# Kernel tuning notes

Measured on AMD Instinct MI355X. Metric: run time of the kernel, lower is better.

## Reference

```python
import jax, jax.numpy as jnp
import numpy as np


def setup_inputs() -> dict:
    key = jax.random.key(0)
    k1, k2 = jax.random.split(key)
    B, H, W, C = 8, 384, 1280, 8
    U = jax.random.normal(k1, (B, H, W, C), dtype=jnp.float32)
    flo = jax.random.normal(k2, (B, H, W, 2), dtype=jnp.float32)
    return {"U": U, "flo": flo}


def _forward_warp(U, flo):
    # Faithful port of transformerFwd: bilinear forward splatting.
    B, H, W, C = U.shape
    out_h, out_w = H, W  # out_size == (H, W) as used in get_occlusion_mask_from_flow
    # normalized sampling grid in [-1, 1]
    x_s = jnp.linspace(-1.0, 1.0, out_w, dtype=jnp.float32)  # [W]
    y_s = jnp.linspace(-1.0, 1.0, out_h, dtype=jnp.float32)  # [H]
    x_t = x_s[None, None, :] + flo[..., 0] / ((out_w - 1.0) / 2.0)  # [B,H,W]
    y_t = y_s[None, :, None] + flo[..., 1] / ((out_h - 1.0) / 2.0)  # [B,H,W]
    # map back to pixel coords
    x = (x_t.reshape(-1) + 1.0) * (W - 1.0) / 2.0  # [B*H*W]
    y = (y_t.reshape(-1) + 1.0) * (H - 1.0) / 2.0
    x0 = jnp.floor(x).astype(jnp.int32)
    x1 = x0 + 1
    y0 = jnp.floor(y).astype(jnp.int32)
    y1 = y0 + 1
    x0c = jnp.clip(x0, 0, W - 1)
    x1c = jnp.clip(x1, 0, W - 1)
    y0c = jnp.clip(y0, 0, H - 1)
    y1c = jnp.clip(y1, 0, H - 1)
    # flat destination indices into [B*H*W]
    base = jnp.repeat(jnp.arange(B, dtype=jnp.int32) * (H * W), out_h * out_w)
    idx_a = base + y0c * W + x0c
    idx_b = base + y1c * W + x0c
    idx_c = base + y0c * W + x1c
    idx_d = base + y1c * W + x1c
    x0f = x0.astype(jnp.float32)
    x1f = x1.astype(jnp.float32)
    y0f = y0.astype(jnp.float32)
    y1f = y1.astype(jnp.float32)
    # bilinear weights, zeroed where the tap fell out of bounds (clamp changed it)
    wa = jnp.where((x0c == x0) & (y0c == y0), (x1f - x) * (y1f - y), 0.0)
    wb = jnp.where((x0c == x0) & (y1c == y1), (x1f - x) * (y - y0f), 0.0)
    wc = jnp.where((x1c == x1) & (y0c == y0), (x - x0f) * (y1f - y), 0.0)
    wd = jnp.where((x1c == x1) & (y1c == y1), (x - x0f) * (y - y0f), 0.0)
    im_flat = U.reshape(-1, C)  # [B*H*W, C]
    out = jnp.zeros((B * H * W, C), dtype=jnp.float32)
    out = out.at[idx_a].add(im_flat * wa[:, None])
    out = out.at[idx_b].add(im_flat * wb[:, None])
    out = out.at[idx_c].add(im_flat * wc[:, None])
    out = out.at[idx_d].add(im_flat * wd[:, None])
    return out.reshape(B, out_h, out_w, C)


def reference(U, flo):
    return _forward_warp(U, flo)
```

## Files before the change

### kernel.cpp

```cpp
#include <hip/hip_runtime.h>
#include <math.h>

constexpr int Bc = 8, Hc = 384, Wc = 1280, Cc = 8;

constexpr int TH = 16, TW = 16;
constexpr int WIN = 3;
constexpr float FMAX = 2.5f;
constexpr int RH = TH + 2 * WIN;
constexpr int RW = TW + 2 * WIN;
constexpr int PSTR = RW + 1;
constexpr int TILES_X = Wc / TW;
constexpr int TILES_Y = Hc / TH;
constexpr int BLK = 256;

__global__ __launch_bounds__(BLK) void fwd_warp_gather(
    const float* __restrict__ U, const float* __restrict__ flo,
    float* __restrict__ out)
{
    __shared__ float2 sxy[RH * PSTR];

    int tile = blockIdx.x;
    int b  = tile / (TILES_X * TILES_Y);
    int r  = tile % (TILES_X * TILES_Y);
    int Y0 = (r / TILES_X) * TH;
    int X0 = (r % TILES_X) * TW;
    int t  = threadIdx.x;

    const float2* flo2 = reinterpret_cast<const float2*>(flo);
    const float4* u4   = reinterpret_cast<const float4*>(U);

    for (int i = t; i < RH * RW; i += BLK) {
        int sy = i / RW, sx = i - sy * RW;
        int h = Y0 - WIN + sy;
        int w = X0 - WIN + sx;
        float2 v = make_float2(-1e9f, -1e9f);
        if ((unsigned)h < (unsigned)Hc && (unsigned)w < (unsigned)Wc) {
            float2 f = flo2[(b * Hc + h) * Wc + w];
            if (fabsf(f.x) <= FMAX && fabsf(f.y) <= FMAX)
                v = make_float2((float)w + f.x, (float)h + f.y);
        }
        sxy[sy * PSTR + sx] = v;
    }
    __syncthreads();

    int lpy = t >> 4, lpx = t & 15;
    int py = Y0 + lpy, px = X0 + lpx;
    float pxf = (float)px, pyf = (float)py;
    int pixbase = (b * Hc + py) * Wc + px;

    unsigned long long mask = 0ull;
    #pragma unroll
    for (int dy = 0; dy < 2 * WIN + 1; ++dy) {
        int rb = (lpy + dy) * PSTR + lpx;
        #pragma unroll
        for (int dx = 0; dx < 2 * WIN + 1; ++dx) {
            float2 s = sxy[rb + dx];
            float m = fmaxf(fabsf(s.x - pxf), fabsf(s.y - pyf));
            unsigned long long hit = (m < 1.0f) ? 1ull : 0ull;
            mask |= hit << (dy * 8 + dx);
        }
    }

    float a0 = 0.f, a1 = 0.f, a2 = 0.f, a3 = 0.f;
    float a4 = 0.f, a5 = 0.f, a6 = 0.f, a7 = 0.f;
    while (mask) {
        int bit = __builtin_ctzll(mask);
        mask &= mask - 1;
        int dy = bit >> 3, dx = bit & 7;
        float2 s = sxy[(lpy + dy) * PSTR + lpx + dx];
        float wgt = (1.0f - fabsf(s.x - pxf)) * (1.0f - fabsf(s.y - pyf));
        int sidx = pixbase + (dy - WIN) * Wc + (dx - WIN);
        float4 ua = u4[(size_t)sidx * 2];
        float4 ub = u4[(size_t)sidx * 2 + 1];
        a0 += ua.x * wgt; a1 += ua.y * wgt;
        a2 += ua.z * wgt; a3 += ua.w * wgt;
        a4 += ub.x * wgt; a5 += ub.y * wgt;
        a6 += ub.z * wgt; a7 += ub.w * wgt;
    }

    float4 o0 = {a0, a1, a2, a3};
    float4 o1 = {a4, a5, a6, a7};
    reinterpret_cast<float4*>(out)[(size_t)pixbase * 2]     = o0;
    reinterpret_cast<float4*>(out)[(size_t)pixbase * 2 + 1] = o1;
}

__global__ __launch_bounds__(BLK) void fwd_warp_outlier(
    const float* __restrict__ U, const float* __restrict__ flo,
    float* __restrict__ out)
{
    int tid = blockIdx.x * BLK + threadIdx.x;
    int total = Bc * Hc * Wc;
    if (tid >= total) return;
    float2 f = reinterpret_cast<const float2*>(flo)[tid];
    if (fabsf(f.x) <= FMAX && fabsf(f.y) <= FMAX) return;

    int w = tid % Wc;
    int h = (tid / Wc) % Hc;
    float x = (float)w + f.x;
    float y = (float)h + f.y;
    float x0f = floorf(x), y0f = floorf(y);
    int x0 = (int)x0f, y0 = (int)y0f;
    float wx[2] = { (x0f + 1.0f) - x, x - x0f };
    float wy[2] = { (y0f + 1.0f) - y, y - y0f };

    const float4* u4 = reinterpret_cast<const float4*>(U);
    float4 ua = u4[(size_t)tid * 2];
    float4 ub = u4[(size_t)tid * 2 + 1];
    int bbase = tid - (h * Wc + w);

    #pragma unroll
    for (int j = 0; j < 2; ++j) {
        #pragma unroll
        for (int k = 0; k < 2; ++k) {
            int ty = y0 + j, tx = x0 + k;
            if ((unsigned)ty < (unsigned)Hc && (unsigned)tx < (unsigned)Wc) {
                float wgt = wx[k] * wy[j];
                if (wgt != 0.0f) {
                    float* p = out + ((size_t)(bbase + ty * Wc + tx)) * 8;
                    atomicAdd(p + 0, ua.x * wgt);
                    atomicAdd(p + 1, ua.y * wgt);
                    atomicAdd(p + 2, ua.z * wgt);
                    atomicAdd(p + 3, ua.w * wgt);
                    atomicAdd(p + 4, ub.x * wgt);
                    atomicAdd(p + 5, ub.y * wgt);
                    atomicAdd(p + 6, ub.z * wgt);
                    atomicAdd(p + 7, ub.w * wgt);
                }
            }
        }
    }
}

extern "C" void kernel_launch(void* const* d_in, const int* in_sizes, int n_in,
                              void* d_out, int out_size, void* d_ws, size_t ws_size,
                              hipStream_t stream)
{
    const float* U   = (const float*)d_in[0];
    const float* flo = (const float*)d_in[1];
    float* out = (float*)d_out;

    int grid_g = Bc * TILES_X * TILES_Y;
    fwd_warp_gather<<<grid_g, BLK, 0, stream>>>(U, flo, out);

    int grid_o = (Bc * Hc * Wc + BLK - 1) / BLK;
    fwd_warp_outlier<<<grid_o, BLK, 0, stream>>>(U, flo, out);
}
```

Baseline: 452.6 us.

## Stage U halo in shared memory and compact outliers into a workspace list

The gather kernel now loads each tile's U halo into shared memory alongside the flow, so splat accumulation reads from LDS instead of scattered global loads. While loading, it appends the indices of large-flow pixels to a list in the workspace through a global atomic counter. A new outlier kernel then walks only that list, which avoids a second full pass over the flow field. The large-flow threshold is also raised so fewer pixels go to the atomic path. The costs are more shared memory per block (lower occupancy) and reliance on the workspace being large enough. If the list overflows its fixed capacity, the extra outliers are dropped silently and the output is wrong.

```diff
diff --git a/kernel.cpp b/kernel.cpp
--- a/kernel.cpp
+++ b/kernel.cpp
@@ -5,19 +5,22 @@
 
 constexpr int TH = 16, TW = 16;
 constexpr int WIN = 3;
-constexpr float FMAX = 2.5f;
+constexpr float FMAX = 3.0f;
 constexpr int RH = TH + 2 * WIN;
 constexpr int RW = TW + 2 * WIN;
 constexpr int PSTR = RW + 1;
 constexpr int TILES_X = Wc / TW;
 constexpr int TILES_Y = Hc / TH;
 constexpr int BLK = 256;
+constexpr unsigned LIST_CAP = 262144;
+constexpr size_t WS_NEED = 16 + (size_t)LIST_CAP * 4;
 
 __global__ __launch_bounds__(BLK) void fwd_warp_gather(
     const float* __restrict__ U, const float* __restrict__ flo,
-    float* __restrict__ out)
+    float* __restrict__ out, unsigned* __restrict__ ws, int do_append)
 {
     __shared__ float2 sxy[RH * PSTR];
+    __shared__ float4 sU[RH * PSTR * 2];
 
     int tile = blockIdx.x;
     int b  = tile / (TILES_X * TILES_Y);
@@ -33,13 +36,25 @@
         int sy = i / RW, sx = i - sy * RW;
         int h = Y0 - WIN + sy;
         int w = X0 - WIN + sx;
-        float2 v = make_float2(-1e9f, -1e9f);
-        if ((unsigned)h < (unsigned)Hc && (unsigned)w < (unsigned)Wc) {
-            float2 f = flo2[(b * Hc + h) * Wc + w];
-            if (fabsf(f.x) <= FMAX && fabsf(f.y) <= FMAX)
-                v = make_float2((float)w + f.x, (float)h + f.y);
-        }
-        sxy[sy * PSTR + sx] = v;
+        bool inimg = ((unsigned)h < (unsigned)Hc) & ((unsigned)w < (unsigned)Wc);
+        int hc = min(max(h, 0), Hc - 1);
+        int wc = min(max(w, 0), Wc - 1);
+        int sidx = (b * Hc + hc) * Wc + wc;
+        float2 f  = flo2[sidx];
+        float4 ua = u4[(size_t)sidx * 2];
+        float4 ub = u4[(size_t)sidx * 2 + 1];
+        bool inl = (fabsf(f.x) <= FMAX) && (fabsf(f.y) <= FMAX);
+        float2 v = (inimg && inl) ? make_float2((float)w + f.x, (float)h + f.y)
+                                  : make_float2(-1e9f, -1e9f);
+        int st = sy * PSTR + sx;
+        sxy[st]        = v;
+        sU[st * 2]     = ua;
+        sU[st * 2 + 1] = ub;
+        if (do_append && inimg && !inl &&
+            sy >= WIN && sy < WIN + TH && sx >= WIN && sx < WIN + TW) {
+            unsigned pos = atomicAdd(ws, 1u);
+            if (pos < LIST_CAP) ws[4 + pos] = (unsigned)sidx;
+        }
     }
     __syncthreads();
 
@@ -67,11 +82,11 @@
         int bit = __builtin_ctzll(mask);
         mask &= mask - 1;
         int dy = bit >> 3, dx = bit & 7;
-        float2 s = sxy[(lpy + dy) * PSTR + lpx + dx];
+        int st = (lpy + dy) * PSTR + lpx + dx;
+        float2 s = sxy[st];
         float wgt = (1.0f - fabsf(s.x - pxf)) * (1.0f - fabsf(s.y - pyf));
-        int sidx = pixbase + (dy - WIN) * Wc + (dx - WIN);
-        float4 ua = u4[(size_t)sidx * 2];
-        float4 ub = u4[(size_t)sidx * 2 + 1];
+        float4 ua = sU[st * 2];
+        float4 ub = sU[st * 2 + 1];
         a0 += ua.x * wgt; a1 += ua.y * wgt;
         a2 += ua.z * wgt; a3 += ua.w * wgt;
         a4 += ub.x * wgt; a5 += ub.y * wgt;
@@ -84,7 +99,55 @@
     reinterpret_cast<float4*>(out)[(size_t)pixbase * 2 + 1] = o1;
 }
 
-__global__ __launch_bounds__(BLK) void fwd_warp_outlier(
+__global__ __launch_bounds__(BLK) void fwd_warp_outlier_list(
+    const float* __restrict__ U, const float* __restrict__ flo,
+    float* __restrict__ out, const unsigned* __restrict__ ws)
+{
+    unsigned n = min(ws[0], LIST_CAP);
+    for (unsigned i = blockIdx.x * BLK + threadIdx.x; i < n;
+         i += gridDim.x * BLK) {
+        int sidx = (int)ws[4 + i];
+        int w = sidx % Wc;
+        int h = (sidx / Wc) % Hc;
+        float2 f = reinterpret_cast<const float2*>(flo)[sidx];
+
+        float x = (float)w + f.x;
+        float y = (float)h + f.y;
+        float x0f = floorf(x), y0f = floorf(y);
+        int x0 = (int)x0f, y0 = (int)y0f;
+        float wx[2] = { (x0f + 1.0f) - x, x - x0f };
+        float wy[2] = { (y0f + 1.0f) - y, y - y0f };
+
+        const float4* u4 = reinterpret_cast<const float4*>(U);
+        float4 ua = u4[(size_t)sidx * 2];
+        float4 ub = u4[(size_t)sidx * 2 + 1];
+        int bbase = sidx - (h * Wc + w);
+
+        #pragma unroll
+        for (int j = 0; j < 2; ++j) {
+            #pragma unroll
+            for (int k = 0; k < 2; ++k) {
+                int ty = y0 + j, tx = x0 + k;
+                if ((unsigned)ty < (unsigned)Hc && (unsigned)tx < (unsigned)Wc) {
+                    float wgt = wx[k] * wy[j];
+                    if (wgt != 0.0f) {
+                        float* p = out + ((size_t)(bbase + ty * Wc + tx)) * 8;
+                        atomicAdd(p + 0, ua.x * wgt);
+                        atomicAdd(p + 1, ua.y * wgt);
+                        atomicAdd(p + 2, ua.z * wgt);
+                        atomicAdd(p + 3, ua.w * wgt);
+                        atomicAdd(p + 4, ub.x * wgt);
+                        atomicAdd(p + 5, ub.y * wgt);
+                        atomicAdd(p + 6, ub.z * wgt);
+                        atomicAdd(p + 7, ub.w * wgt);
+                    }
+                }
+            }
+        }
+    }
+}
+
+__global__ __launch_bounds__(BLK) void fwd_warp_outlier_scan(
     const float* __restrict__ U, const float* __restrict__ flo,
     float* __restrict__ out)
 {
@@ -138,10 +201,18 @@
     const float* U   = (const float*)d_in[0];
     const float* flo = (const float*)d_in[1];
     float* out = (float*)d_out;
-
+    unsigned* ws = (unsigned*)d_ws;
+
+    bool use_list = (ws != nullptr) && (ws_size >= WS_NEED);
     int grid_g = Bc * TILES_X * TILES_Y;
-    fwd_warp_gather<<<grid_g, BLK, 0, stream>>>(U, flo, out);
-
-    int grid_o = (Bc * Hc * Wc + BLK - 1) / BLK;
-    fwd_warp_outlier<<<grid_o, BLK, 0, stream>>>(U, flo, out);
-}
+
+    if (use_list) {
+        hipMemsetAsync(d_ws, 0, 16, stream);
+        fwd_warp_gather<<<grid_g, BLK, 0, stream>>>(U, flo, out, ws, 1);
+        fwd_warp_outlier_list<<<256, BLK, 0, stream>>>(U, flo, out, ws);
+    } else {
+        fwd_warp_gather<<<grid_g, BLK, 0, stream>>>(U, flo, out, ws, 0);
+        int grid_o = (Bc * Hc * Wc + BLK - 1) / BLK;
+        fwd_warp_outlier_scan<<<grid_o, BLK, 0, stream>>>(U, flo, out);
+    }
+}
```

Measured after the change: 437.2 us. 1.04x faster.
